# Kernel optimization log

Hardware: AMD Instinct MI355X
Metric: run time of the kernel (lower is better)

Reference implementation:

```python
import jax, jax.numpy as jnp
import numpy as np

HIDDEN = 4096
N_EXPERTS = 128
TOP_K = 8
N_GROUP = 8
TOPK_GROUP = 4
ROUTED_SCALE = 1.0
NORM_TOPK = True
T = 32768


def setup_inputs() -> dict:
    key = jax.random.key(0)
    k1, k2, k3 = jax.random.split(key, 3)
    hidden_states = jax.random.normal(k1, (T, HIDDEN), dtype=jnp.float32)
    weight = jax.random.normal(k2, (N_EXPERTS, HIDDEN), dtype=jnp.float32) * 0.02
    e_score_correction_bias = jax.random.normal(k3, (N_EXPERTS,), dtype=jnp.float32) * 0.1
    return {"hidden_states": hidden_states, "weight": weight,
            "e_score_correction_bias": e_score_correction_bias}


def reference(hidden_states, weight, e_score_correction_bias):
    # GLM4-MoE top-k router: linear -> sigmoid -> bias-corrected grouped top-k
    x = hidden_states.reshape(-1, HIDDEN)
    router_logits = jnp.einsum('th,eh->te', x, weight)          # [T, E]
    scores = jax.nn.sigmoid(router_logits)                      # [T, E]
    scores_for_choice = scores + e_score_correction_bias[None, :]

    per_group = N_EXPERTS // N_GROUP
    g = scores_for_choice.reshape(-1, N_GROUP, per_group)       # [T, G, E/G]
    # group score = sum of top-2 expert scores within each group
    group_scores = jax.lax.top_k(g, 2)[0].sum(axis=-1)          # [T, G]
    group_idx = jax.lax.top_k(group_scores, TOPK_GROUP)[1]      # [T, topk_group]
    group_mask = jax.nn.one_hot(group_idx, N_GROUP, dtype=scores.dtype).sum(axis=1)  # [T, G]
    score_mask = jnp.repeat(group_mask, per_group, axis=-1)     # [T, E]
    masked_scores = jnp.where(score_mask > 0, scores_for_choice, 0.0)

    topk_indices = jax.lax.top_k(masked_scores, TOP_K)[1]       # [T, top_k]
    topk_weights = jnp.take_along_axis(scores, topk_indices, axis=1)  # gather raw (un-biased) scores
    if NORM_TOPK:
        denom = topk_weights.sum(axis=-1, keepdims=True) + 1e-20
        topk_weights = topk_weights / denom
    topk_weights = topk_weights * ROUTED_SCALE
    return topk_indices, topk_weights
```

## Files before the change

### kernel.cpp

```cpp
#include <hip/hip_runtime.h>
#include <math.h>

#define T_TOKENS 32768
#define HIDDEN   4096
#define NEXP     128
#define TM       64
#define BK       32
#define NSTAGE   (HIDDEN / BK)

#define A_BUF_SH      6144
#define B_BASE_SH     (2 * A_BUF_SH)
#define B_BUF_SH      12288
#define LDS_SHORTS    (B_BASE_SH + 2 * B_BUF_SH)
#define B_BASE_BYTES  (B_BASE_SH * 2)
#define B_BUF_BYTES   (B_BUF_SH * 2)
#define A_PLANE_SH    2048
#define B_PLANE_SH    4096
#define SC_STRIDE     129
#define B_CHUNK_BYTES B_BUF_BYTES
#define WS_BYTES ((size_t)NSTAGE * B_CHUNK_BYTES)

typedef short bf16x8 __attribute__((ext_vector_type(8)));
typedef short bf16x4 __attribute__((ext_vector_type(4)));
typedef float f32x4  __attribute__((ext_vector_type(4)));

__device__ __forceinline__ unsigned short f2bf(float f) {
    unsigned u = __float_as_uint(f);
    u += 0x7FFF + ((u >> 16) & 1);
    return (unsigned short)(u >> 16);
}
__device__ __forceinline__ float bf2f(unsigned short h) {
    return __uint_as_float(((unsigned)h) << 16);
}
__device__ __forceinline__ void split3(float x, unsigned short& b0,
                                       unsigned short& b1, unsigned short& b2) {
    b0 = f2bf(x);
    float r1 = x - bf2f(b0);
    b1 = f2bf(r1);
    float r2 = r1 - bf2f(b1);
    b2 = f2bf(r2);
}

__global__ __launch_bounds__(256) void presplit_w(
    const float* __restrict__ w, short* __restrict__ ws16)
{
    const int g = blockIdx.x * 256 + threadIdx.x;
    const int l = g & 63;
    const int t = (g >> 6) & 7;
    const int s = g >> 9;
    const int e  = t * 16 + (l & 15);
    const int kb = s * BK + ((l >> 4) & 3) * 8;
    const float* src = w + (size_t)e * HIDDEN + kb;
    float4 v0 = *(const float4*)(src);
    float4 v1 = *(const float4*)(src + 4);
    float vv[8] = {v0.x, v0.y, v0.z, v0.w, v1.x, v1.y, v1.z, v1.w};
    unsigned short h0[8], h1[8], h2[8];
#pragma unroll
    for (int j = 0; j < 8; ++j) split3(vv[j], h0[j], h1[j], h2[j]);
    const size_t base = ((size_t)s * 24 + t) * 64 + l;
    bf16x8 o0 = {(short)h0[0],(short)h0[1],(short)h0[2],(short)h0[3],
                 (short)h0[4],(short)h0[5],(short)h0[6],(short)h0[7]};
    bf16x8 o1 = {(short)h1[0],(short)h1[1],(short)h1[2],(short)h1[3],
                 (short)h1[4],(short)h1[5],(short)h1[6],(short)h1[7]};
    bf16x8 o2 = {(short)h2[0],(short)h2[1],(short)h2[2],(short)h2[3],
                 (short)h2[4],(short)h2[5],(short)h2[6],(short)h2[7]};
    *(bf16x8*)(ws16 + (base + 0 * 8 * 64) * 8) = o0;
    *(bf16x8*)(ws16 + (base + 1 * 8 * 64) * 8) = o1;
    *(bf16x8*)(ws16 + (base + 2 * 8 * 64) * 8) = o2;
}

__global__ __launch_bounds__(512, 4) void glm4_router_mfma(
    const float* __restrict__ x, const short* __restrict__ wsplit,
    const float* __restrict__ bias, float* __restrict__ out)
{
    __shared__ __align__(16) short lds[LDS_SHORTS];

    const int tid  = threadIdx.x;
    const int wid  = tid >> 6;
    const int lane = tid & 63;
    const int rt_base = (wid & 1) * 2;
    const int ct_base = (wid >> 1) * 2;
    const int tok_base = blockIdx.x * TM;

    const int al = (tid >> 1) & 63;
    const int at = tid >> 7;
    const int arow = at * 16 + (al & 15);
    const int akoff = ((al >> 4) & 3) * 8 + (tid & 1) * 4;
    const float* xsrc = x + (size_t)(tok_base + arow) * HIDDEN + akoff;
    const int awr = tid * 4;

    f32x4 acc[2][2];
    double accd[2][2][4];
#pragma unroll
    for (int r = 0; r < 2; ++r)
#pragma unroll
        for (int c = 0; c < 2; ++c) {
            acc[r][c] = (f32x4){0.f, 0.f, 0.f, 0.f};
#pragma unroll
            for (int v = 0; v < 4; ++v) accd[r][c][v] = 0.0;
        }

#define GLDS_B(S, BUF) do {                                                    \
    const char* gsrc_ = (const char*)wsplit + (size_t)(S) * B_CHUNK_BYTES + tid * 16; \
    char* ldst_ = (char*)lds + B_BASE_BYTES + (BUF) * B_BUF_BYTES + tid * 16;  \
    __builtin_amdgcn_global_load_lds(                                          \
        (const __attribute__((address_space(1))) unsigned*)(gsrc_),            \
        (__attribute__((address_space(3))) unsigned*)(ldst_), 16, 0, 0);       \
    __builtin_amdgcn_global_load_lds(                                          \
        (const __attribute__((address_space(1))) unsigned*)(gsrc_ + 8192),     \
        (__attribute__((address_space(3))) unsigned*)(ldst_ + 8192), 16, 0, 0);\
    __builtin_amdgcn_global_load_lds(                                          \
        (const __attribute__((address_space(1))) unsigned*)(gsrc_ + 16384),    \
        (__attribute__((address_space(3))) unsigned*)(ldst_ + 16384), 16, 0, 0);\
} while (0)

#define SPLIT_A(XV, BUF) do {                                                  \
    unsigned short h0_[4], h1_[4], h2_[4];                                     \
    split3((XV).x, h0_[0], h1_[0], h2_[0]);                                    \
    split3((XV).y, h0_[1], h1_[1], h2_[1]);                                    \
    split3((XV).z, h0_[2], h1_[2], h2_[2]);                                    \
    split3((XV).w, h0_[3], h1_[3], h2_[3]);                                    \
    short* ab_ = &lds[(BUF) * A_BUF_SH + awr];                                 \
    *(bf16x4*)(ab_ + 0 * A_PLANE_SH) =                                         \
        (bf16x4){(short)h0_[0], (short)h0_[1], (short)h0_[2], (short)h0_[3]};  \
    *(bf16x4*)(ab_ + 1 * A_PLANE_SH) =                                         \
        (bf16x4){(short)h1_[0], (short)h1_[1], (short)h1_[2], (short)h1_[3]};  \
    *(bf16x4*)(ab_ + 2 * A_PLANE_SH) =                                         \
        (bf16x4){(short)h2_[0], (short)h2_[1], (short)h2_[2], (short)h2_[3]};  \
} while (0)

#define COMPUTE(S, BUF) do {                                                   \
    bf16x8 Af[3][2], Bf[3][2];                                                 \
    _Pragma("unroll")                                                          \
    for (int p = 0; p < 3; ++p) {                                              \
        _Pragma("unroll")                                                      \
        for (int r = 0; r < 2; ++r)                                            \
            Af[p][r] = *(const bf16x8*)(&lds[(BUF) * A_BUF_SH + p * A_PLANE_SH \
                                             + ((rt_base + r) * 64 + lane) * 8]); \
        _Pragma("unroll")                                                      \
        for (int c = 0; c < 2; ++c)                                            \
            Bf[p][c] = *(const bf16x8*)(&lds[B_BASE_SH + (BUF) * B_BUF_SH      \
                                             + p * B_PLANE_SH                  \
                                             + ((ct_base + c) * 64 + lane) * 8]); \
    }                                                                          \
    _Pragma("unroll")                                                          \
    for (int r = 0; r < 2; ++r) {                                              \
        _Pragma("unroll")                                                      \
        for (int c = 0; c < 2; ++c) {                                          \
            acc[r][c] = __builtin_amdgcn_mfma_f32_16x16x32_bf16(Af[0][r], Bf[0][c], acc[r][c], 0, 0, 0); \
            acc[r][c] = __builtin_amdgcn_mfma_f32_16x16x32_bf16(Af[0][r], Bf[1][c], acc[r][c], 0, 0, 0); \
            acc[r][c] = __builtin_amdgcn_mfma_f32_16x16x32_bf16(Af[1][r], Bf[0][c], acc[r][c], 0, 0, 0); \
            acc[r][c] = __builtin_amdgcn_mfma_f32_16x16x32_bf16(Af[0][r], Bf[2][c], acc[r][c], 0, 0, 0); \
            acc[r][c] = __builtin_amdgcn_mfma_f32_16x16x32_bf16(Af[2][r], Bf[0][c], acc[r][c], 0, 0, 0); \
            acc[r][c] = __builtin_amdgcn_mfma_f32_16x16x32_bf16(Af[1][r], Bf[1][c], acc[r][c], 0, 0, 0); \
        }                                                                      \
    }                                                                          \
    if (((S) & 3) == 3) {                                                      \
        _Pragma("unroll")                                                      \
        for (int r = 0; r < 2; ++r)                                            \
            _Pragma("unroll")                                                  \
            for (int c = 0; c < 2; ++c) {                                      \
                _Pragma("unroll")                                              \
                for (int v = 0; v < 4; ++v) accd[r][c][v] += (double)acc[r][c][v]; \
                acc[r][c] = (f32x4){0.f, 0.f, 0.f, 0.f};                       \
            }                                                                  \
    }                                                                          \
} while (0)

    float4 xA, xB;
    {
        float4 x0v = *(const float4*)(xsrc);
        GLDS_B(0, 0);
        xA = *(const float4*)(xsrc + BK);
        SPLIT_A(x0v, 0);
    }
    __syncthreads();

#define BODY(S, BUF, XC, XL) do {                                              \
    GLDS_B((S) + 1, (BUF) ^ 1);                                                \
    {                                                                          \
        int s2_ = (S) + 2; if (s2_ > NSTAGE - 1) s2_ = NSTAGE - 1;             \
        XL = *(const float4*)(xsrc + (size_t)s2_ * BK);                        \
    }                                                                          \
    SPLIT_A(XC, (BUF) ^ 1);                                                    \
    COMPUTE(S, BUF);                                                           \
    __syncthreads();                                                           \
} while (0)

    for (int s = 0; s < NSTAGE - 2; s += 2) {
        BODY(s, 0, xA, xB);
        BODY(s + 1, 1, xB, xA);
    }
    BODY(NSTAGE - 2, 0, xA, xB);
    COMPUTE(NSTAGE - 1, 1);

    __syncthreads();
    float* sc = (float*)lds;
#pragma unroll
    for (int r = 0; r < 2; ++r)
#pragma unroll
        for (int c = 0; c < 2; ++c) {
#pragma unroll
            for (int v = 0; v < 4; ++v) {
                const int tokl = (rt_base + r) * 16 + (lane >> 4) * 4 + v;
                const int e    = (ct_base + c) * 16 + (lane & 15);
                const float lg = (float)accd[r][c][v];
                const float sg = (float)(1.0 / (1.0 + exp(-(double)lg)));
                sc[tokl * SC_STRIDE + e] = sg + bias[e];
            }
        }
    __syncthreads();

    if (tid < TM) {
        const float* scp = sc + tid * SC_STRIDE;

        float gsc[8];
#pragma unroll
        for (int g = 0; g < 8; ++g) {
            float m1 = -1e30f, m2 = -1e30f;
#pragma unroll
            for (int j = 0; j < 16; ++j) {
                const float v = scp[g * 16 + j];
                if (v > m1) { m2 = m1; m1 = v; }
                else if (v > m2) { m2 = v; }
            }
            gsc[g] = m1 + m2;
        }

        unsigned gmask = 0;
#pragma unroll
        for (int p = 0; p < 4; ++p) {
            float best = -1e30f; int bi = 0;
#pragma unroll
            for (int g = 0; g < 8; ++g) {
                const bool taken = (gmask >> g) & 1u;
                if (!taken && gsc[g] > best) { best = gsc[g]; bi = g; }
            }
            gmask |= 1u << bi;
        }

        unsigned long long chosen0 = 0ull, chosen1 = 0ull;
        int   idxs[8];
        float wts[8];
#pragma unroll
        for (int p = 0; p < 8; ++p) {
            float best = -1e30f; int bi = 0;
            for (int e = 0; e < NEXP; ++e) {
                const bool sel = (gmask >> (e >> 4)) & 1u;
                const float v = sel ? scp[e] : 0.0f;
                const bool ch = (e < 64) ? ((chosen0 >> e) & 1ull)
                                         : ((chosen1 >> (e - 64)) & 1ull);
                if (!ch && v > best) { best = v; bi = e; }
            }
            if (bi < 64) chosen0 |= 1ull << bi; else chosen1 |= 1ull << (bi - 64);
            idxs[p] = bi;
            wts[p] = scp[bi] - bias[bi];
        }

        float denom = 0.0f;
#pragma unroll
        for (int p = 0; p < 8; ++p) denom += wts[p];
        denom += 1e-20f;

        const size_t row = (size_t)(tok_base + tid) * 8;
        float* outI = out;
        float* outW = out + (size_t)T_TOKENS * 8;
#pragma unroll
        for (int p = 0; p < 8; ++p) {
            outI[row + p] = (float)idxs[p];
            outW[row + p] = wts[p] / denom;
        }
    }
}

extern "C" void kernel_launch(void* const* d_in, const int* in_sizes, int n_in,
                              void* d_out, int out_size, void* d_ws, size_t ws_size,
                              hipStream_t stream) {
    const float* x    = (const float*)d_in[0];
    const float* w    = (const float*)d_in[1];
    const float* bias = (const float*)d_in[2];
    float* out = (float*)d_out;
    short* ws16 = (short*)d_ws;

    presplit_w<<<dim3(NSTAGE * 8 * 64 / 256), 256, 0, stream>>>(w, ws16);
    glm4_router_mfma<<<dim3(T_TOKENS / TM), 512, 0, stream>>>(x, ws16, bias, out);
}
```

Measured before the change: 282.3 us.

## Load pre-split weight fragments straight from global memory into registers

Drops the LDS staging of the three-way bf16-split weight operand, which used async global-to-LDS copies. Each wave now reads its MFMA B fragments directly from the pre-laid-out workspace in global memory, and only the activation split stays double-buffered in LDS. LDS use shrinks to the size of the epilogue score buffer, which should allow more resident blocks and makes the per-stage barrier lighter. The cost is that B fragment loads now have global/L2 latency right before the MFMAs, and every wave fetches its own fragments, so there is no shared LDS copy.

```diff
diff --git a/kernel.cpp b/kernel.cpp
--- a/kernel.cpp
+++ b/kernel.cpp
@@ -9,16 +9,11 @@
 #define NSTAGE   (HIDDEN / BK)
 
 #define A_BUF_SH      6144
-#define B_BASE_SH     (2 * A_BUF_SH)
-#define B_BUF_SH      12288
-#define LDS_SHORTS    (B_BASE_SH + 2 * B_BUF_SH)
-#define B_BASE_BYTES  (B_BASE_SH * 2)
-#define B_BUF_BYTES   (B_BUF_SH * 2)
 #define A_PLANE_SH    2048
-#define B_PLANE_SH    4096
 #define SC_STRIDE     129
-#define B_CHUNK_BYTES B_BUF_BYTES
-#define WS_BYTES ((size_t)NSTAGE * B_CHUNK_BYTES)
+#define LDS_SHORTS    16512
+#define B_CHUNK_SH    12288
+#define WS_BYTES ((size_t)NSTAGE * B_CHUNK_SH * 2)
 
 typedef short bf16x8 __attribute__((ext_vector_type(8)));
 typedef short bf16x4 __attribute__((ext_vector_type(4)));
@@ -89,6 +84,8 @@
     const float* xsrc = x + (size_t)(tok_base + arow) * HIDDEN + akoff;
     const int awr = tid * 4;
 
+    const short* wfrag = wsplit + (size_t)lane * 8;
+
     f32x4 acc[2][2];
     double accd[2][2][4];
 #pragma unroll
@@ -99,20 +96,6 @@
 #pragma unroll
             for (int v = 0; v < 4; ++v) accd[r][c][v] = 0.0;
         }
-
-#define GLDS_B(S, BUF) do {                                                    \
-    const char* gsrc_ = (const char*)wsplit + (size_t)(S) * B_CHUNK_BYTES + tid * 16; \
-    char* ldst_ = (char*)lds + B_BASE_BYTES + (BUF) * B_BUF_BYTES + tid * 16;  \
-    __builtin_amdgcn_global_load_lds(                                          \
-        (const __attribute__((address_space(1))) unsigned*)(gsrc_),            \
-        (__attribute__((address_space(3))) unsigned*)(ldst_), 16, 0, 0);       \
-    __builtin_amdgcn_global_load_lds(                                          \
-        (const __attribute__((address_space(1))) unsigned*)(gsrc_ + 8192),     \
-        (__attribute__((address_space(3))) unsigned*)(ldst_ + 8192), 16, 0, 0);\
-    __builtin_amdgcn_global_load_lds(                                          \
-        (const __attribute__((address_space(1))) unsigned*)(gsrc_ + 16384),    \
-        (__attribute__((address_space(3))) unsigned*)(ldst_ + 16384), 16, 0, 0);\
-} while (0)
 
 #define SPLIT_A(XV, BUF) do {                                                  \
     unsigned short h0_[4], h1_[4], h2_[4];                                     \
@@ -129,20 +112,33 @@
         (bf16x4){(short)h2_[0], (short)h2_[1], (short)h2_[2], (short)h2_[3]};  \
 } while (0)
 
-#define COMPUTE(S, BUF) do {                                                   \
-    bf16x8 Af[3][2], Bf[3][2];                                                 \
+#define A_BARRIER() do {                                                       \
+    asm volatile("s_waitcnt lgkmcnt(0)" ::: "memory");                         \
+    __builtin_amdgcn_s_barrier();                                              \
+    __builtin_amdgcn_sched_barrier(0);                                         \
+} while (0)
+
+#define BODY(S, BUF, XC, XL) do {                                              \
+    bf16x8 Bf[3][2];                                                           \
     _Pragma("unroll")                                                          \
     for (int p = 0; p < 3; ++p) {                                              \
+        _Pragma("unroll")                                                      \
+        for (int c = 0; c < 2; ++c)                                            \
+            Bf[p][c] = *(const bf16x8*)(                                       \
+                wfrag + ((size_t)(S) * 24 + p * 8 + ct_base + c) * 512);       \
+    }                                                                          \
+    {                                                                          \
+        int s2_ = (S) + 2; if (s2_ > NSTAGE - 1) s2_ = NSTAGE - 1;             \
+        XL = *(const float4*)(xsrc + (size_t)s2_ * BK);                        \
+    }                                                                          \
+    SPLIT_A(XC, (BUF) ^ 1);                                                    \
+    bf16x8 Af[3][2];                                                           \
+    _Pragma("unroll")                                                          \
+    for (int p = 0; p < 3; ++p)                                                \
         _Pragma("unroll")                                                      \
         for (int r = 0; r < 2; ++r)                                            \
             Af[p][r] = *(const bf16x8*)(&lds[(BUF) * A_BUF_SH + p * A_PLANE_SH \
                                              + ((rt_base + r) * 64 + lane) * 8]); \
-        _Pragma("unroll")                                                      \
-        for (int c = 0; c < 2; ++c)                                            \
-            Bf[p][c] = *(const bf16x8*)(&lds[B_BASE_SH + (BUF) * B_BUF_SH      \
-                                             + p * B_PLANE_SH                  \
-                                             + ((ct_base + c) * 64 + lane) * 8]); \
-    }                                                                          \
     _Pragma("unroll")                                                          \
     for (int r = 0; r < 2; ++r) {                                              \
         _Pragma("unroll")                                                      \
@@ -165,34 +161,61 @@
                 acc[r][c] = (f32x4){0.f, 0.f, 0.f, 0.f};                       \
             }                                                                  \
     }                                                                          \
+    A_BARRIER();                                                               \
 } while (0)
 
     float4 xA, xB;
     {
         float4 x0v = *(const float4*)(xsrc);
-        GLDS_B(0, 0);
         xA = *(const float4*)(xsrc + BK);
+        SPLIT_A(x0v, 1);
+    }
+    {
+        float4 x0v = *(const float4*)(xsrc);
         SPLIT_A(x0v, 0);
     }
-    __syncthreads();
-
-#define BODY(S, BUF, XC, XL) do {                                              \
-    GLDS_B((S) + 1, (BUF) ^ 1);                                                \
-    {                                                                          \
-        int s2_ = (S) + 2; if (s2_ > NSTAGE - 1) s2_ = NSTAGE - 1;             \
-        XL = *(const float4*)(xsrc + (size_t)s2_ * BK);                        \
-    }                                                                          \
-    SPLIT_A(XC, (BUF) ^ 1);                                                    \
-    COMPUTE(S, BUF);                                                           \
-    __syncthreads();                                                           \
-} while (0)
+    A_BARRIER();
 
     for (int s = 0; s < NSTAGE - 2; s += 2) {
         BODY(s, 0, xA, xB);
         BODY(s + 1, 1, xB, xA);
     }
     BODY(NSTAGE - 2, 0, xA, xB);
-    COMPUTE(NSTAGE - 1, 1);
+
+    {
+        const int S = NSTAGE - 1;
+        bf16x8 Bf[3][2];
+#pragma unroll
+        for (int p = 0; p < 3; ++p)
+#pragma unroll
+            for (int c = 0; c < 2; ++c)
+                Bf[p][c] = *(const bf16x8*)(
+                    wfrag + ((size_t)S * 24 + p * 8 + ct_base + c) * 512);
+        bf16x8 Af[3][2];
+#pragma unroll
+        for (int p = 0; p < 3; ++p)
+#pragma unroll
+            for (int r = 0; r < 2; ++r)
+                Af[p][r] = *(const bf16x8*)(&lds[1 * A_BUF_SH + p * A_PLANE_SH
+                                                 + ((rt_base + r) * 64 + lane) * 8]);
+#pragma unroll
+        for (int r = 0; r < 2; ++r)
+#pragma unroll
+            for (int c = 0; c < 2; ++c) {
+                acc[r][c] = __builtin_amdgcn_mfma_f32_16x16x32_bf16(Af[0][r], Bf[0][c], acc[r][c], 0, 0, 0);
+                acc[r][c] = __builtin_amdgcn_mfma_f32_16x16x32_bf16(Af[0][r], Bf[1][c], acc[r][c], 0, 0, 0);
+                acc[r][c] = __builtin_amdgcn_mfma_f32_16x16x32_bf16(Af[1][r], Bf[0][c], acc[r][c], 0, 0, 0);
+                acc[r][c] = __builtin_amdgcn_mfma_f32_16x16x32_bf16(Af[0][r], Bf[2][c], acc[r][c], 0, 0, 0);
+                acc[r][c] = __builtin_amdgcn_mfma_f32_16x16x32_bf16(Af[2][r], Bf[0][c], acc[r][c], 0, 0, 0);
+                acc[r][c] = __builtin_amdgcn_mfma_f32_16x16x32_bf16(Af[1][r], Bf[1][c], acc[r][c], 0, 0, 0);
+            }
+#pragma unroll
+        for (int r = 0; r < 2; ++r)
+#pragma unroll
+            for (int c = 0; c < 2; ++c)
+#pragma unroll
+                for (int v = 0; v < 4; ++v) accd[r][c][v] += (double)acc[r][c][v];
+    }
 
     __syncthreads();
     float* sc = (float*)lds;
```

Result: slower. 288.0 us (+2.0%).

## Switch router GEMM to 32x32x16 MFMA tiles with interleaved A-split

Applied to the files above, without the earlier changes.

Replaces the four 16x16x32 MFMA accumulators per wave with a single 32x32x16 tile, re-laying out the presplit weight and the A fragments in LDS to match. The A split for the next stage is placed between the two k-halves of MFMA work, and s_setprio is raised around the MFMA bursts. The goal is fewer LDS fragment reads per FLOP and better overlap of VALU split work with matrix ops. The cost is larger per-instruction latency and a more intricate lane-to-token mapping in the epilogue.

```diff
diff --git a/kernel.cpp b/kernel.cpp
--- a/kernel.cpp
+++ b/kernel.cpp
@@ -15,14 +15,13 @@
 #define B_BASE_BYTES  (B_BASE_SH * 2)
 #define B_BUF_BYTES   (B_BUF_SH * 2)
 #define A_PLANE_SH    2048
-#define B_PLANE_SH    4096
 #define SC_STRIDE     129
 #define B_CHUNK_BYTES B_BUF_BYTES
 #define WS_BYTES ((size_t)NSTAGE * B_CHUNK_BYTES)
 
 typedef short bf16x8 __attribute__((ext_vector_type(8)));
 typedef short bf16x4 __attribute__((ext_vector_type(4)));
-typedef float f32x4  __attribute__((ext_vector_type(4)));
+typedef float f32x16 __attribute__((ext_vector_type(16)));
 
 __device__ __forceinline__ unsigned short f2bf(float f) {
     unsigned u = __float_as_uint(f);
@@ -44,12 +43,13 @@
 __global__ __launch_bounds__(256) void presplit_w(
     const float* __restrict__ w, short* __restrict__ ws16)
 {
-    const int g = blockIdx.x * 256 + threadIdx.x;
-    const int l = g & 63;
-    const int t = (g >> 6) & 7;
-    const int s = g >> 9;
-    const int e  = t * 16 + (l & 15);
-    const int kb = s * BK + ((l >> 4) & 3) * 8;
+    const int g  = blockIdx.x * 256 + threadIdx.x;
+    const int l  = g & 63;
+    const int t  = (g >> 6) & 3;
+    const int kk = (g >> 8) & 1;
+    const int s  = g >> 9;
+    const int e  = t * 32 + (l & 31);
+    const int kb = s * BK + kk * 16 + ((l >> 5) & 1) * 8;
     const float* src = w + (size_t)e * HIDDEN + kb;
     float4 v0 = *(const float4*)(src);
     float4 v1 = *(const float4*)(src + 4);
@@ -57,16 +57,16 @@
     unsigned short h0[8], h1[8], h2[8];
 #pragma unroll
     for (int j = 0; j < 8; ++j) split3(vv[j], h0[j], h1[j], h2[j]);
-    const size_t base = ((size_t)s * 24 + t) * 64 + l;
+    const size_t fb = ((size_t)(s * 2 + kk) * 12 + t) * 64 + l;
     bf16x8 o0 = {(short)h0[0],(short)h0[1],(short)h0[2],(short)h0[3],
                  (short)h0[4],(short)h0[5],(short)h0[6],(short)h0[7]};
     bf16x8 o1 = {(short)h1[0],(short)h1[1],(short)h1[2],(short)h1[3],
                  (short)h1[4],(short)h1[5],(short)h1[6],(short)h1[7]};
     bf16x8 o2 = {(short)h2[0],(short)h2[1],(short)h2[2],(short)h2[3],
                  (short)h2[4],(short)h2[5],(short)h2[6],(short)h2[7]};
-    *(bf16x8*)(ws16 + (base + 0 * 8 * 64) * 8) = o0;
-    *(bf16x8*)(ws16 + (base + 1 * 8 * 64) * 8) = o1;
-    *(bf16x8*)(ws16 + (base + 2 * 8 * 64) * 8) = o2;
+    *(bf16x8*)(ws16 + (fb + 0 * 4 * 64) * 8) = o0;
+    *(bf16x8*)(ws16 + (fb + 1 * 4 * 64) * 8) = o1;
+    *(bf16x8*)(ws16 + (fb + 2 * 4 * 64) * 8) = o2;
 }
 
 __global__ __launch_bounds__(512, 4) void glm4_router_mfma(
@@ -78,27 +78,20 @@
     const int tid  = threadIdx.x;
     const int wid  = tid >> 6;
     const int lane = tid & 63;
-    const int rt_base = (wid & 1) * 2;
-    const int ct_base = (wid >> 1) * 2;
+    const int rt   = wid & 1;
+    const int ct   = wid >> 1;
     const int tok_base = blockIdx.x * TM;
 
-    const int al = (tid >> 1) & 63;
-    const int at = tid >> 7;
-    const int arow = at * 16 + (al & 15);
-    const int akoff = ((al >> 4) & 3) * 8 + (tid & 1) * 4;
+    const int af   = tid >> 1;
+    const int arow = (af >> 7) * 32 + (af & 31);
+    const int akoff = (((af >> 6) & 1) * 16) + (((af >> 5) & 1) * 8) + (tid & 1) * 4;
     const float* xsrc = x + (size_t)(tok_base + arow) * HIDDEN + akoff;
     const int awr = tid * 4;
 
-    f32x4 acc[2][2];
-    double accd[2][2][4];
-#pragma unroll
-    for (int r = 0; r < 2; ++r)
-#pragma unroll
-        for (int c = 0; c < 2; ++c) {
-            acc[r][c] = (f32x4){0.f, 0.f, 0.f, 0.f};
-#pragma unroll
-            for (int v = 0; v < 4; ++v) accd[r][c][v] = 0.0;
-        }
+    f32x16 acc;
+    double accd[16];
+#pragma unroll
+    for (int v = 0; v < 16; ++v) { acc[v] = 0.0f; accd[v] = 0.0; }
 
 #define GLDS_B(S, BUF) do {                                                    \
     const char* gsrc_ = (const char*)wsplit + (size_t)(S) * B_CHUNK_BYTES + tid * 16; \
@@ -129,42 +122,43 @@
         (bf16x4){(short)h2_[0], (short)h2_[1], (short)h2_[2], (short)h2_[3]};  \
 } while (0)
 
-#define COMPUTE(S, BUF) do {                                                   \
-    bf16x8 Af[3][2], Bf[3][2];                                                 \
-    _Pragma("unroll")                                                          \
-    for (int p = 0; p < 3; ++p) {                                              \
-        _Pragma("unroll")                                                      \
-        for (int r = 0; r < 2; ++r)                                            \
-            Af[p][r] = *(const bf16x8*)(&lds[(BUF) * A_BUF_SH + p * A_PLANE_SH \
-                                             + ((rt_base + r) * 64 + lane) * 8]); \
-        _Pragma("unroll")                                                      \
-        for (int c = 0; c < 2; ++c)                                            \
-            Bf[p][c] = *(const bf16x8*)(&lds[B_BASE_SH + (BUF) * B_BUF_SH      \
-                                             + p * B_PLANE_SH                  \
-                                             + ((ct_base + c) * 64 + lane) * 8]); \
+#define MFMA_K(BUF, KK) do {                                                   \
+    bf16x8 a0 = *(const bf16x8*)(&lds[(BUF) * A_BUF_SH + 0 * A_PLANE_SH        \
+                                      + ((rt * 2 + (KK)) * 64 + lane) * 8]);   \
+    bf16x8 a1 = *(const bf16x8*)(&lds[(BUF) * A_BUF_SH + 1 * A_PLANE_SH        \
+                                      + ((rt * 2 + (KK)) * 64 + lane) * 8]);   \
+    bf16x8 a2 = *(const bf16x8*)(&lds[(BUF) * A_BUF_SH + 2 * A_PLANE_SH        \
+                                      + ((rt * 2 + (KK)) * 64 + lane) * 8]);   \
+    bf16x8 b0 = *(const bf16x8*)(&lds[B_BASE_SH + (BUF) * B_BUF_SH             \
+                                      + (((KK) * 12 + 0 * 4 + ct) * 64 + lane) * 8]); \
+    bf16x8 b1 = *(const bf16x8*)(&lds[B_BASE_SH + (BUF) * B_BUF_SH             \
+                                      + (((KK) * 12 + 1 * 4 + ct) * 64 + lane) * 8]); \
+    bf16x8 b2 = *(const bf16x8*)(&lds[B_BASE_SH + (BUF) * B_BUF_SH             \
+                                      + (((KK) * 12 + 2 * 4 + ct) * 64 + lane) * 8]); \
+    __builtin_amdgcn_s_setprio(1);                                             \
+    acc = __builtin_amdgcn_mfma_f32_32x32x16_bf16(a0, b0, acc, 0, 0, 0);       \
+    acc = __builtin_amdgcn_mfma_f32_32x32x16_bf16(a0, b1, acc, 0, 0, 0);       \
+    acc = __builtin_amdgcn_mfma_f32_32x32x16_bf16(a1, b0, acc, 0, 0, 0);       \
+    acc = __builtin_amdgcn_mfma_f32_32x32x16_bf16(a0, b2, acc, 0, 0, 0);       \
+    acc = __builtin_amdgcn_mfma_f32_32x32x16_bf16(a2, b0, acc, 0, 0, 0);       \
+    acc = __builtin_amdgcn_mfma_f32_32x32x16_bf16(a1, b1, acc, 0, 0, 0);       \
+    __builtin_amdgcn_s_setprio(0);                                             \
+} while (0)
+
+#define BODY(S, BUF, XC, XL) do {                                              \
+    GLDS_B((S) + 1, (BUF) ^ 1);                                                \
+    {                                                                          \
+        int s2_ = (S) + 2; if (s2_ > NSTAGE - 1) s2_ = NSTAGE - 1;             \
+        XL = *(const float4*)(xsrc + (size_t)s2_ * BK);                        \
     }                                                                          \
-    _Pragma("unroll")                                                          \
-    for (int r = 0; r < 2; ++r) {                                              \
-        _Pragma("unroll")                                                      \
-        for (int c = 0; c < 2; ++c) {                                          \
-            acc[r][c] = __builtin_amdgcn_mfma_f32_16x16x32_bf16(Af[0][r], Bf[0][c], acc[r][c], 0, 0, 0); \
-            acc[r][c] = __builtin_amdgcn_mfma_f32_16x16x32_bf16(Af[0][r], Bf[1][c], acc[r][c], 0, 0, 0); \
-            acc[r][c] = __builtin_amdgcn_mfma_f32_16x16x32_bf16(Af[1][r], Bf[0][c], acc[r][c], 0, 0, 0); \
-            acc[r][c] = __builtin_amdgcn_mfma_f32_16x16x32_bf16(Af[0][r], Bf[2][c], acc[r][c], 0, 0, 0); \
-            acc[r][c] = __builtin_amdgcn_mfma_f32_16x16x32_bf16(Af[2][r], Bf[0][c], acc[r][c], 0, 0, 0); \
-            acc[r][c] = __builtin_amdgcn_mfma_f32_16x16x32_bf16(Af[1][r], Bf[1][c], acc[r][c], 0, 0, 0); \
-        }                                                                      \
-    }                                                                          \
+    MFMA_K(BUF, 0);                                                            \
+    SPLIT_A(XC, (BUF) ^ 1);         \
+    MFMA_K(BUF, 1);                                                            \
     if (((S) & 3) == 3) {                                                      \
         _Pragma("unroll")                                                      \
-        for (int r = 0; r < 2; ++r)                                            \
-            _Pragma("unroll")                                                  \
-            for (int c = 0; c < 2; ++c) {                                      \
-                _Pragma("unroll")                                              \
-                for (int v = 0; v < 4; ++v) accd[r][c][v] += (double)acc[r][c][v]; \
-                acc[r][c] = (f32x4){0.f, 0.f, 0.f, 0.f};                       \
-            }                                                                  \
+        for (int v = 0; v < 16; ++v) { accd[v] += (double)acc[v]; acc[v] = 0.0f; } \
     }                                                                          \
+    __syncthreads();       \
 } while (0)
 
     float4 xA, xB;
@@ -176,39 +170,27 @@
     }
     __syncthreads();
 
-#define BODY(S, BUF, XC, XL) do {                                              \
-    GLDS_B((S) + 1, (BUF) ^ 1);                                                \
-    {                                                                          \
-        int s2_ = (S) + 2; if (s2_ > NSTAGE - 1) s2_ = NSTAGE - 1;             \
-        XL = *(const float4*)(xsrc + (size_t)s2_ * BK);                        \
-    }                                                                          \
-    SPLIT_A(XC, (BUF) ^ 1);                                                    \
-    COMPUTE(S, BUF);                                                           \
-    __syncthreads();                                                           \
-} while (0)
-
     for (int s = 0; s < NSTAGE - 2; s += 2) {
         BODY(s, 0, xA, xB);
         BODY(s + 1, 1, xB, xA);
     }
     BODY(NSTAGE - 2, 0, xA, xB);
-    COMPUTE(NSTAGE - 1, 1);
+
+    MFMA_K(1, 0);
+    MFMA_K(1, 1);
+#pragma unroll
+    for (int v = 0; v < 16; ++v) accd[v] += (double)acc[v];
 
     __syncthreads();
     float* sc = (float*)lds;
 #pragma unroll
-    for (int r = 0; r < 2; ++r)
-#pragma unroll
-        for (int c = 0; c < 2; ++c) {
-#pragma unroll
-            for (int v = 0; v < 4; ++v) {
-                const int tokl = (rt_base + r) * 16 + (lane >> 4) * 4 + v;
-                const int e    = (ct_base + c) * 16 + (lane & 15);
-                const float lg = (float)accd[r][c][v];
-                const float sg = (float)(1.0 / (1.0 + exp(-(double)lg)));
-                sc[tokl * SC_STRIDE + e] = sg + bias[e];
-            }
-        }
+    for (int v = 0; v < 16; ++v) {
+        const int tokl = rt * 32 + (v & 3) + 8 * (v >> 2) + 4 * (lane >> 5);
+        const int e    = ct * 32 + (lane & 31);
+        const float lg = (float)accd[v];
+        const float sg = (float)(1.0 / (1.0 + exp(-(double)lg)));
+        sc[tokl * SC_STRIDE + e] = sg + bias[e];
+    }
     __syncthreads();
 
     if (tid < TM) {
@@ -282,6 +264,6 @@
     float* out = (float*)d_out;
     short* ws16 = (short*)d_ws;
 
-    presplit_w<<<dim3(NSTAGE * 8 * 64 / 256), 256, 0, stream>>>(w, ws16);
+    presplit_w<<<dim3(NSTAGE * 2 * 4 * 64 / 256), 256, 0, stream>>>(w, ws16);
     glm4_router_mfma<<<dim3(T_TOKENS / TM), 512, 0, stream>>>(x, ws16, bias, out);
 }
```

Result: slower. 292.4 us (+3.6%).
